# Performance work log

Measured on AMD Instinct MI355X. Metric: run time of the kernel, lower is better.

Reference implementation:

```python
import jax, jax.numpy as jnp
import numpy as np

B, T, C = 2, 2048, 2048
H, KV, D = 16, 4, 128   # n_head, n_kv_head, head_dim
EPS = 1.1920929e-07     # torch.finfo(float32).eps, F.rms_norm default


def setup_inputs() -> dict:
    key = jax.random.key(0)
    ks = jax.random.split(key, 7)
    x = jax.random.normal(ks[0], (B, T, C), dtype=jnp.float32)
    # rope angles: cos/sin of positions, broadcastable to [B,T,H,D//2]
    inv_freq = 1.0 / (10000.0 ** (jnp.arange(0, D // 2, dtype=jnp.float32) / (D // 2)))
    ang = jnp.arange(T, dtype=jnp.float32)[:, None] * inv_freq[None, :]
    cos = jnp.cos(ang)[None, :, None, :]  # [1,T,1,D/2]
    sin = jnp.sin(ang)[None, :, None, :]
    s = 0.02
    Wq = jax.random.normal(ks[1], (C, H * D), dtype=jnp.float32) * s
    Wk = jax.random.normal(ks[2], (C, KV * D), dtype=jnp.float32) * s
    Wv = jax.random.normal(ks[3], (C, KV * D), dtype=jnp.float32) * s
    Wo = jax.random.normal(ks[4], (C, C), dtype=jnp.float32) * s
    return {"x": x, "cos": cos, "sin": sin, "Wq": Wq, "Wk": Wk, "Wv": Wv, "Wo": Wo}


def _rope(t, cos, sin):
    d = t.shape[-1] // 2
    t1, t2 = t[..., :d], t[..., d:]
    return jnp.concatenate([t1 * cos + t2 * sin, -t1 * sin + t2 * cos], axis=-1)


def _rmsnorm(t):
    return t * jax.lax.rsqrt(jnp.mean(t * t, axis=-1, keepdims=True) + EPS)


def reference(x, cos, sin, Wq, Wk, Wv, Wo):
    q = (x @ Wq).reshape(B, T, H, D)
    k = (x @ Wk).reshape(B, T, KV, D)
    v = (x @ Wv).reshape(B, T, KV, D)
    q = _rmsnorm(_rope(q, cos, sin))
    k = _rmsnorm(_rope(k, cos, sin))
    # [B, KV, G, T, D] query grouped per kv head (GQA)
    G = H // KV
    qh = q.transpose(0, 2, 1, 3).reshape(B, KV, G, T, D)
    kh = k.transpose(0, 2, 1, 3)  # [B, KV, T, D]
    vh = v.transpose(0, 2, 1, 3)
    scale = 1.0 / np.sqrt(D).astype(np.float32)
    scores = jnp.einsum('bhgqd,bhkd->bhgqk', qh, kh) * scale
    causal = jnp.tril(jnp.ones((T, T), dtype=bool))
    scores = jnp.where(causal, scores, jnp.finfo(scores.dtype).min)
    attn = jax.nn.softmax(scores, axis=-1)
    y = jnp.einsum('bhgqk,bhkd->bhgqd', attn, vh)  # [B,KV,G,T,D]
    y = y.reshape(B, H, T, D).transpose(0, 2, 1, 3).reshape(B, T, C)
    return y @ Wo
```

## Files before the change

### kernel.cpp

```cpp
#include <hip/hip_runtime.h>

using bf16x8 = __attribute__((ext_vector_type(8))) short;
using f32x4  = __attribute__((ext_vector_type(4))) float;

#define B_  2
#define T_  2048
#define C_  2048
#define H_  16
#define KV_ 4
#define D_  128

__device__ __forceinline__ unsigned short f2b(float f) {
  union { float f; unsigned int u; } v; v.f = f;
  unsigned int r = v.u + 0x7fffu + ((v.u >> 16) & 1u);
  return (unsigned short)(r >> 16);
}
__device__ __forceinline__ float b2f(unsigned short u) {
  union { unsigned int u; float f; } v; v.u = ((unsigned int)u) << 16;
  return v.f;
}
__device__ __forceinline__ unsigned int cvt_pk_bf16(float lo, float hi) {
  unsigned int r;
  asm("v_cvt_pk_bf16_f32 %0, %1, %2" : "=v"(r) : "v"(lo), "v"(hi));
  return r;
}
__device__ __forceinline__ void gld_lds16(const void* g, void* l) {
  __builtin_amdgcn_global_load_lds(
      (__attribute__((address_space(1))) void*)g,
      (__attribute__((address_space(3))) void*)l, 16, 0, 0);
}

__global__ void cast_bf16_k(const float* __restrict__ in, unsigned short* __restrict__ out) {
  int i = blockIdx.x * 256 + threadIdx.x;
  float4 f = ((const float4*)in)[i];
  ushort4 u; u.x = f2b(f.x); u.y = f2b(f.y); u.z = f2b(f.z); u.w = f2b(f.w);
  ((ushort4*)out)[i] = u;
}

__global__ void wtrans4(const float* __restrict__ Wq, const float* __restrict__ Wk,
                        const float* __restrict__ Wv, const float* __restrict__ Wo,
                        unsigned short* __restrict__ Wqt, unsigned short* __restrict__ Wkt,
                        unsigned short* __restrict__ Wvt, unsigned short* __restrict__ Wot) {
  __shared__ float s[32][33];
  int id = blockIdx.x;
  const float* W; unsigned short* Wt; int N;
  if (id < 4096)      { W = Wq; Wt = Wqt; N = 2048; }
  else if (id < 5120) { W = Wk; Wt = Wkt; N = 512;  id -= 4096; }
  else if (id < 6144) { W = Wv; Wt = Wvt; N = 512;  id -= 5120; }
  else                { W = Wo; Wt = Wot; N = 2048; id -= 6144; }
  int ntiles = N >> 5;
  int n0 = (id % ntiles) * 32, k0 = (id / ntiles) * 32;
  int tx = threadIdx.x, ty = threadIdx.y;
  #pragma unroll
  for (int yy = 0; yy < 32; yy += 8)
    s[ty + yy][tx] = W[(size_t)(k0 + ty + yy) * N + n0 + tx];
  __syncthreads();
  #pragma unroll
  for (int yy = 0; yy < 32; yy += 8)
    Wt[(size_t)(n0 + ty + yy) * 2048 + k0 + tx] = f2b(s[tx][ty + yy]);
}

template <bool OUT_BF16>
__device__ __forceinline__ void gemm_tile(
    const unsigned short* __restrict__ A, const unsigned short* __restrict__ Bt,
    void* __restrict__ Cv, int K, int ldc, int m0, int n0b, int n0c,
    unsigned short* sA, unsigned short* sB)
{
  const int tid  = threadIdx.x;
  const int lane = tid & 63, w = tid >> 6;
  const int quad = lane >> 4, l16 = lane & 15;
  const int wm = (w >> 1) * 64, wn = (w & 1) * 64;

  f32x4 acc[4][4] = {};

  const unsigned short* Abase = A  + (size_t)m0  * K;
  const unsigned short* Bbase = Bt + (size_t)n0b * K;

  for (int k0 = 0; k0 < K; k0 += 32) {
    #pragma unroll
    for (int r = 0; r < 2; ++r) {
      int c = tid + r * 256;
      int row = c >> 2, col = (c & 3) * 8;
      gld_lds16(Abase + (size_t)row * K + k0 + col, sA + c * 8);
      gld_lds16(Bbase + (size_t)row * K + k0 + col, sB + c * 8);
    }
    __syncthreads();
    bf16x8 af[4], bfr[4];
    #pragma unroll
    for (int i = 0; i < 4; ++i)
      af[i]  = *(const bf16x8*)(sA + (wm + i * 16 + l16) * 32 + quad * 8);
    #pragma unroll
    for (int j = 0; j < 4; ++j)
      bfr[j] = *(const bf16x8*)(sB + (wn + j * 16 + l16) * 32 + quad * 8);
    #pragma unroll
    for (int i = 0; i < 4; ++i)
      #pragma unroll
      for (int j = 0; j < 4; ++j)
        acc[i][j] = __builtin_amdgcn_mfma_f32_16x16x32_bf16(af[i], bfr[j], acc[i][j], 0, 0, 0);
    __syncthreads();
  }
  #pragma unroll
  for (int i = 0; i < 4; ++i) {
    #pragma unroll
    for (int r = 0; r < 4; ++r) {
      int row = m0 + wm + i * 16 + quad * 4 + r;
      #pragma unroll
      for (int j = 0; j < 4; ++j) {
        int col = n0c + wn + j * 16 + l16;
        float v = acc[i][j][r];
        if (OUT_BF16) ((unsigned short*)Cv)[(size_t)row * ldc + col] = f2b(v);
        else          ((float*)Cv)[(size_t)row * ldc + col] = v;
      }
    }
  }
}

__global__ void out_gemm(const unsigned short* __restrict__ yb,
                         const unsigned short* __restrict__ Wot,
                         float* __restrict__ out) {
  __shared__ unsigned short sA[128 * 32], sB[128 * 32];
  gemm_tile<false>(yb, Wot, out, C_, C_, blockIdx.y * 128, blockIdx.x * 128, blockIdx.x * 128,
                   sA, sB);
}

__global__ __launch_bounds__(512, 2) void qkv_gemm8(
    const unsigned short* __restrict__ xb,
    const unsigned short* __restrict__ Wqt,
    const unsigned short* __restrict__ Wkt,
    const unsigned short* __restrict__ Wvt,
    unsigned short* __restrict__ q, unsigned short* __restrict__ k,
    unsigned short* __restrict__ v) {
  __shared__ unsigned short lds[65536];

  const int id  = (int)blockIdx.x;
  const int xcd = id & 7, jj = id >> 3;
  const int mt  = xcd * 2 + jj / 12;
  const int nt  = jj % 12;

  const unsigned short* Bt; unsigned short* Cp; int n0, ldc;
  if (nt < 8)       { Bt = Wqt; Cp = q; n0 = nt * 256;        ldc = 2048; }
  else if (nt < 10) { Bt = Wkt; Cp = k; n0 = (nt - 8) * 256;  ldc = 512;  }
  else              { Bt = Wvt; Cp = v; n0 = (nt - 10) * 256; ldc = 512;  }
  const int m0 = mt * 256;

  const int tid = (int)threadIdx.x;
  const int w = tid >> 6, lane = tid & 63;
  const int quad = lane >> 4, l16 = lane & 15;
  const int wr = w >> 2, wc = w & 3;
  const int swz = (l16 & 12) << 1;

  const unsigned short* Ab = xb + (size_t)m0 * 2048;
  const unsigned short* Bb = Bt + (size_t)n0 * 2048;

  const int c0 = tid, c1 = tid + 512;
  const int r0 = c0 >> 2, r1 = c1 >> 2;
  const int x0 = ((c0 & 3) * 8) ^ (((c0 >> 4) & 3) << 3);
  const int x1 = ((c1 & 3) * 8) ^ (((c1 >> 4) & 3) << 3);

#define STAGE_A(buf, kh, kb) do { \
    unsigned short* d_ = lds + (buf) * 16384 + (kh) * 8192; \
    gld_lds16(Ab + (size_t)r0 * 2048 + (kb) + (kh) * 32 + x0, d_ + c0 * 8); \
    gld_lds16(Ab + (size_t)r1 * 2048 + (kb) + (kh) * 32 + x1, d_ + c1 * 8); \
  } while (0)
#define STAGE_B(buf, kh, kb) do { \
    unsigned short* d_ = lds + 32768 + (buf) * 16384 + (kh) * 8192; \
    gld_lds16(Bb + (size_t)r0 * 2048 + (kb) + (kh) * 32 + x0, d_ + c0 * 8); \
    gld_lds16(Bb + (size_t)r1 * 2048 + (kb) + (kh) * 32 + x1, d_ + c1 * 8); \
  } while (0)

  f32x4 acc[8][4] = {};

  STAGE_A(0, 0, 0); STAGE_B(0, 0, 0); STAGE_A(0, 1, 0); STAGE_B(0, 1, 0);
  asm volatile("s_waitcnt vmcnt(4)" ::: "memory");
  __builtin_amdgcn_s_barrier();

  const unsigned short* aLd = lds + (wr * 128 + l16) * 32 + (quad * 8 ^ swz);
  const unsigned short* bLd = lds + 32768 + (wc * 64 + l16) * 32 + (quad * 8 ^ swz);

  for (int t = 0; t < 32; ++t) {
    const int cur = t & 1, nxt = cur ^ 1;
    const bool more = (t < 31);
    const int kb = (t + 1) * 64;
    const int off = cur * 16384;
    bf16x8 a[8], bbr[4];

    #pragma unroll
    for (int m = 0; m < 8; ++m) a[m] = *(const bf16x8*)(aLd + off + m * 512);
    #pragma unroll
    for (int n = 0; n < 4; ++n) bbr[n] = *(const bf16x8*)(bLd + off + n * 512);
    if (more) {
      STAGE_A(nxt, 0, kb); STAGE_B(nxt, 0, kb);
      STAGE_A(nxt, 1, kb); STAGE_B(nxt, 1, kb);
    }
    asm volatile("s_waitcnt lgkmcnt(0)" ::: "memory");
    __builtin_amdgcn_sched_barrier(0);
    __builtin_amdgcn_s_setprio(1);
    #pragma unroll
    for (int m = 0; m < 8; ++m)
      #pragma unroll
      for (int n = 0; n < 4; ++n)
        acc[m][n] = __builtin_amdgcn_mfma_f32_16x16x32_bf16(a[m], bbr[n], acc[m][n], 0, 0, 0);
    __builtin_amdgcn_s_setprio(0);
    if (more) asm volatile("s_waitcnt vmcnt(8)" ::: "memory");
    else      asm volatile("s_waitcnt vmcnt(0)" ::: "memory");
    __builtin_amdgcn_s_barrier();

    #pragma unroll
    for (int m = 0; m < 8; ++m) a[m] = *(const bf16x8*)(aLd + off + 8192 + m * 512);
    #pragma unroll
    for (int n = 0; n < 4; ++n) bbr[n] = *(const bf16x8*)(bLd + off + 8192 + n * 512);
    asm volatile("s_waitcnt lgkmcnt(0)" ::: "memory");
    __builtin_amdgcn_sched_barrier(0);
    __builtin_amdgcn_s_setprio(1);
    #pragma unroll
    for (int m = 0; m < 8; ++m)
      #pragma unroll
      for (int n = 0; n < 4; ++n)
        acc[m][n] = __builtin_amdgcn_mfma_f32_16x16x32_bf16(a[m], bbr[n], acc[m][n], 0, 0, 0);
    __builtin_amdgcn_s_setprio(0);
    if (more) asm volatile("s_waitcnt vmcnt(4)" ::: "memory");
    else      asm volatile("s_waitcnt vmcnt(0)" ::: "memory");
    __builtin_amdgcn_s_barrier();
  }
#undef STAGE_A
#undef STAGE_B

  #pragma unroll
  for (int m = 0; m < 8; ++m)
    #pragma unroll
    for (int r = 0; r < 4; ++r) {
      int row = m0 + wr * 128 + m * 16 + quad * 4 + r;
      #pragma unroll
      for (int n = 0; n < 4; ++n) {
        int col = n0 + wc * 64 + n * 16 + l16;
        Cp[(size_t)row * ldc + col] = f2b(acc[m][n][r]);
      }
    }
}

template <int NH>
__global__ void ropenorm(const unsigned short* __restrict__ in,
                         const float* __restrict__ cs, const float* __restrict__ sn,
                         unsigned short* __restrict__ out, float oscale) {
  int row  = blockIdx.x * 4 + (threadIdx.x >> 6);
  int lane = threadIdx.x & 63;
  int head = row % NH;
  int t = (row / NH) & (T_ - 1);
  int b = row / (NH * T_);
  const unsigned short* p = in + (size_t)row * D_;
  unsigned int u  = *(const unsigned int*)(p + 2 * lane);
  unsigned int up = (unsigned int)__shfl_xor((int)u, 32, 64);
  int dh = (lane & 31) * 2;
  float2 c2 = ((const float2*)(cs + t * 64))[lane & 31];
  float2 s2 = ((const float2*)(sn + t * 64))[lane & 31];
  float a0 = b2f((unsigned short)(u & 0xffff)),  a1 = b2f((unsigned short)(u >> 16));
  float p0 = b2f((unsigned short)(up & 0xffff)), p1 = b2f((unsigned short)(up >> 16));
  float sgn = (lane < 32) ? 1.0f : -1.0f;
  float oa = a0 * c2.x + sgn * p0 * s2.x;
  float ob = a1 * c2.y + sgn * p1 * s2.y;
  float ss = oa * oa + ob * ob;
  #pragma unroll
  for (int off = 32; off > 0; off >>= 1) ss += __shfl_xor(ss, off, 64);
  float r = rsqrtf(ss * (1.0f / 128.0f) + 1.1920929e-07f) * oscale;
  unsigned int outu = cvt_pk_bf16(oa * r, ob * r);
  size_t base = ((size_t)((b * NH + head) * 128 + (t >> 4))) * 2048 + (size_t)(t & 15) * 8;
  int f = ((lane < 32) ? 0 : 8) + (dh >> 3);
  *(unsigned int*)(out + base + (size_t)f * 128 + (dh & 7)) = outu;
}

__global__ void vfrag_k(const unsigned short* __restrict__ v, unsigned short* __restrict__ vf) {
  int it = blockIdx.x;
  int b = blockIdx.y >> 2, kv = blockIdx.y & 3;
  int d = threadIdx.x, ty = threadIdx.y;
  int t0 = it * 64;
  size_t obase = ((size_t)((b * KV_ + kv) * 32 + it)) * 8192
               + (size_t)(d >> 4) * 1024 + (size_t)(d & 15) * 8;
  #pragma unroll
  for (int tcg = 0; tcg < 4; ++tcg) {
    int tc = ty * 4 + tcg;
    unsigned short val[8];
    #pragma unroll
    for (int e = 0; e < 8; ++e)
      val[e] = v[(((size_t)(b * T_) + t0 + tc * 8 + e) * KV_ + kv) * D_ + d];
    ushort4 u0 = {val[0], val[1], val[2], val[3]};
    ushort4 u1 = {val[4], val[5], val[6], val[7]};
    *(ushort4*)(vf + obase + (size_t)tc * 128)     = u0;
    *(ushort4*)(vf + obase + (size_t)tc * 128 + 4) = u1;
  }
}

__global__ __launch_bounds__(256, 2) void attn_kernel(
    const unsigned short* __restrict__ qf, const unsigned short* __restrict__ kf,
    const unsigned short* __restrict__ vf, unsigned short* __restrict__ yb) {
  __shared__ __align__(16) char smem[34048];

  const int xp = (int)blockIdx.x;
  const int b = xp >> 2, kv = xp & 3;
  const int yp = (int)blockIdx.y;
  const int j = yp >> 2, hp = yp & 3;
  const int tid = threadIdx.x;
  const int w = tid >> 6, lane = tid & 63;
  const int quad = lane >> 4, l16 = lane & 15;
  const int qsel = w & 1, half = w >> 1;
  const int qt = qsel ? (63 - j) : j;
  const int h = kv * 4 + hp;
  const int q0 = qt * 32;
  const int ntile = (qt >> 1) + 1;
  unsigned short* myP = (unsigned short*)smem + w * (32 * 72);

  const unsigned short* Qf = qf + ((size_t)(b * H_ + h) * 128 + qt * 2) * 2048;
  const unsigned short* Kf = kf + (size_t)(b * KV_ + kv) * 128 * 2048;
  const unsigned short* Vf = vf + (size_t)(b * KV_ + kv) * 32 * 8192;

  bf16x8 bq[2][4];
  #pragma unroll
  for (int i = 0; i < 2; ++i)
    #pragma unroll
    for (int kk = 0; kk < 4; ++kk)
      bq[i][kk] = *(const bf16x8*)(Qf + (size_t)i * 2048 + (kk * 4 + quad) * 128 + l16 * 8);

  float l_i[2] = {0.f, 0.f};
  f32x4 o[2][8] = {};

  for (int it = half; it < ntile; it += 2) {
    const int t0 = it * 64;
    const unsigned short* Kt = Kf + (size_t)(it * 4) * 2048;
    const unsigned short* Vt = Vf + (size_t)it * 8192;

    f32x4 sc[4][2] = {};
    #pragma unroll
    for (int kk = 0; kk < 4; ++kk) {
      bf16x8 ak[4];
      #pragma unroll
      for (int jt = 0; jt < 4; ++jt)
        ak[jt] = *(const bf16x8*)(Kt + (size_t)jt * 2048 + (kk * 4 + quad) * 128 + l16 * 8);
      #pragma unroll
      for (int jt = 0; jt < 4; ++jt)
        #pragma unroll
        for (int i = 0; i < 2; ++i)
          sc[jt][i] = __builtin_amdgcn_mfma_f32_16x16x32_bf16(ak[jt], bq[i][kk], sc[jt][i], 0, 0, 0);
    }

    bf16x8 bv[2][8];
    #pragma unroll
    for (int kk2 = 0; kk2 < 2; ++kk2)
      #pragma unroll
      for (int jj = 0; jj < 8; ++jj)
        bv[kk2][jj] = *(const bf16x8*)(Vt + (size_t)jj * 1024 + (kk2 * 4 + quad) * 128 + l16 * 8);

    if (it == ntile - 1) {
      #pragma unroll
      for (int jt = 0; jt < 4; ++jt) {
        int kg = t0 + jt * 16 + quad * 4;
        #pragma unroll
        for (int i = 0; i < 2; ++i) {
          int qg = q0 + i * 16 + l16;
          #pragma unroll
          for (int r = 0; r < 4; ++r)
            if (kg + r > qg) sc[jt][i][r] = -3.0e38f;
        }
      }
    }

    #pragma unroll
    for (int i = 0; i < 2; ++i) {
      float part = 0.f;
      #pragma unroll
      for (int jt = 0; jt < 4; ++jt)
        #pragma unroll
        for (int r = 0; r < 4; ++r) {
          float p = __expf(sc[jt][i][r] - 12.0f);
          sc[jt][i][r] = p; part += p;
        }
      l_i[i] += part;
    }

    #pragma unroll
    for (int i = 0; i < 2; ++i)
      #pragma unroll
      for (int jt = 0; jt < 4; ++jt) {
        uint2 uu;
        uu.x = cvt_pk_bf16(sc[jt][i][0], sc[jt][i][1]);
        uu.y = cvt_pk_bf16(sc[jt][i][2], sc[jt][i][3]);
        *(uint2*)(myP + (i * 16 + l16) * 72 + jt * 16 + quad * 4) = uu;
      }

    #pragma unroll
    for (int kk2 = 0; kk2 < 2; ++kk2) {
      bf16x8 ap[2];
      #pragma unroll
      for (int i = 0; i < 2; ++i)
        ap[i] = *(const bf16x8*)(myP + (i * 16 + l16) * 72 + kk2 * 32 + quad * 8);
      #pragma unroll
      for (int i = 0; i < 2; ++i)
        #pragma unroll
        for (int jj = 0; jj < 8; ++jj)
          o[i][jj] = __builtin_amdgcn_mfma_f32_16x16x32_bf16(ap[i], bv[kk2][jj], o[i][jj], 0, 0, 0);
    }
  }

  float lsum[2];
  #pragma unroll
  for (int i = 0; i < 2; ++i) {
    float l = l_i[i];
    l += __shfl_xor(l, 16, 64);
    l += __shfl_xor(l, 32, 64);
    lsum[i] = l;
  }

  __syncthreads();
  float* oc = (float*)smem + qsel * (32 * 132);
  float* lc = (float*)smem + 2 * (32 * 132) + qsel * 32;
  if (half == 1) {
    #pragma unroll
    for (int i = 0; i < 2; ++i) {
      if (quad == 0) lc[i * 16 + l16] = lsum[i];
      #pragma unroll
      for (int jj = 0; jj < 8; ++jj)
        #pragma unroll
        for (int r = 0; r < 4; ++r)
          oc[(i * 16 + quad * 4 + r) * 132 + jj * 16 + l16] = o[i][jj][r];
    }
  }
  __syncthreads();
  if (half == 0) {
    #pragma unroll
    for (int i = 0; i < 2; ++i) {
      float l = lsum[i] + lc[i * 16 + l16];
      float linv = 1.0f / l;
      float lr[4];
      #pragma unroll
      for (int r = 0; r < 4; ++r) lr[r] = __shfl(linv, quad * 4 + r, 64);
      #pragma unroll
      for (int r = 0; r < 4; ++r) {
        int tg = q0 + i * 16 + quad * 4 + r;
        unsigned short* yr = yb + (((size_t)(b * T_ + tg)) * H_ + h) * D_;
        #pragma unroll
        for (int jj = 0; jj < 8; ++jj) {
          float vsum = o[i][jj][r] + oc[(i * 16 + quad * 4 + r) * 132 + jj * 16 + l16];
          yr[jj * 16 + l16] = f2b(vsum * lr[r]);
        }
      }
    }
  }
}

extern "C" void kernel_launch(void* const* d_in, const int* in_sizes, int n_in,
                              void* d_out, int out_size, void* d_ws, size_t ws_size,
                              hipStream_t stream) {
  (void)in_sizes; (void)n_in; (void)out_size; (void)ws_size;
  const float* x  = (const float*)d_in[0];
  const float* cs = (const float*)d_in[1];
  const float* sn = (const float*)d_in[2];
  const float* Wq = (const float*)d_in[3];
  const float* Wk = (const float*)d_in[4];
  const float* Wv = (const float*)d_in[5];
  const float* Wo = (const float*)d_in[6];
  float* out = (float*)d_out;
  char* ws = (char*)d_ws;

  unsigned short* xb   = (unsigned short*)(ws + 0);
  unsigned short* Wqt  = (unsigned short*)(ws + 16777216);
  unsigned short* Wkt  = (unsigned short*)(ws + 25165824);
  unsigned short* Wvt  = (unsigned short*)(ws + 27262976);
  unsigned short* Wot  = (unsigned short*)(ws + 29360128);
  unsigned short* qraw = (unsigned short*)(ws + 37748736);
  unsigned short* kraw = (unsigned short*)(ws + 54525952);
  unsigned short* vraw = (unsigned short*)(ws + 58720256);
  unsigned short* qfr  = (unsigned short*)(ws + 62914560);
  unsigned short* kfr  = (unsigned short*)(ws + 79691776);
  unsigned short* vfr  = (unsigned short*)(ws + 83886080);
  unsigned short* yb   = qraw;

  cast_bf16_k<<<dim3(8192), dim3(256), 0, stream>>>(x, xb);
  wtrans4<<<dim3(10240), dim3(32, 8), 0, stream>>>(Wq, Wk, Wv, Wo, Wqt, Wkt, Wvt, Wot);
  qkv_gemm8<<<dim3(192), dim3(512), 0, stream>>>(xb, Wqt, Wkt, Wvt, qraw, kraw, vraw);
  ropenorm<16><<<dim3(16384), dim3(256), 0, stream>>>(qraw, cs, sn, qfr, 0.08838834764831845f);
  ropenorm<4><<<dim3(4096),  dim3(256), 0, stream>>>(kraw, cs, sn, kfr, 1.0f);
  vfrag_k<<<dim3(32, 8), dim3(128, 2), 0, stream>>>(vraw, vfr);
  attn_kernel<<<dim3(8, 128), dim3(256), 0, stream>>>(qfr, kfr, vfr, yb);
  out_gemm<<<dim3(16, 32), dim3(256), 0, stream>>>(yb, Wot, out);
}
```

Measured before the change: 318.9 us.

## Fuse QKV weights into one GEMM with 256x192 tiles over 256 blocks

Packs Wq, Wk and Wv transposes contiguously and runs a single QKV GEMM with 256x192 tiles, giving 256 blocks (one full wave on the CUs) instead of 192. The output is one interleaved [B*T, 3072] buffer, so ropenorm and vfrag_k now take a leading dimension and offset. The k-loop is also simplified from hand-tuned split waitcnt/setprio scheduling to a plain double buffer with __syncthreads. This may lose some of the load/compute overlap the manual scheduling provided.

```diff
diff --git a/kernel.cpp b/kernel.cpp
--- a/kernel.cpp
+++ b/kernel.cpp
@@ -123,117 +123,97 @@
                    sA, sB);
 }
 
-__global__ __launch_bounds__(512, 2) void qkv_gemm8(
+__global__ __launch_bounds__(512, 2) void qkv_gemm2p(
     const unsigned short* __restrict__ xb,
-    const unsigned short* __restrict__ Wqt,
-    const unsigned short* __restrict__ Wkt,
-    const unsigned short* __restrict__ Wvt,
-    unsigned short* __restrict__ q, unsigned short* __restrict__ k,
-    unsigned short* __restrict__ v) {
-  __shared__ unsigned short lds[65536];
+    const unsigned short* __restrict__ Wt,
+    unsigned short* __restrict__ qkv) {
+  __shared__ unsigned short lds[57344];
 
   const int id  = (int)blockIdx.x;
-  const int xcd = id & 7, jj = id >> 3;
-  const int mt  = xcd * 2 + jj / 12;
-  const int nt  = jj % 12;
-
-  const unsigned short* Bt; unsigned short* Cp; int n0, ldc;
-  if (nt < 8)       { Bt = Wqt; Cp = q; n0 = nt * 256;        ldc = 2048; }
-  else if (nt < 10) { Bt = Wkt; Cp = k; n0 = (nt - 8) * 256;  ldc = 512;  }
-  else              { Bt = Wvt; Cp = v; n0 = (nt - 10) * 256; ldc = 512;  }
-  const int m0 = mt * 256;
+  const int xcd = id & 7, j = id >> 3;
+  const int mt  = xcd * 2 + (j >> 4);
+  const int nt  = j & 15;
+  const int m0 = mt * 256, n0 = nt * 192;
 
   const int tid = (int)threadIdx.x;
   const int w = tid >> 6, lane = tid & 63;
   const int quad = lane >> 4, l16 = lane & 15;
-  const int wr = w >> 2, wc = w & 3;
+  const int wr = w >> 1, wc = w & 1;
   const int swz = (l16 & 12) << 1;
 
   const unsigned short* Ab = xb + (size_t)m0 * 2048;
-  const unsigned short* Bb = Bt + (size_t)n0 * 2048;
-
-  const int c0 = tid, c1 = tid + 512;
-  const int r0 = c0 >> 2, r1 = c1 >> 2;
-  const int x0 = ((c0 & 3) * 8) ^ (((c0 >> 4) & 3) << 3);
-  const int x1 = ((c1 & 3) * 8) ^ (((c1 >> 4) & 3) << 3);
-
-#define STAGE_A(buf, kh, kb) do { \
-    unsigned short* d_ = lds + (buf) * 16384 + (kh) * 8192; \
-    gld_lds16(Ab + (size_t)r0 * 2048 + (kb) + (kh) * 32 + x0, d_ + c0 * 8); \
-    gld_lds16(Ab + (size_t)r1 * 2048 + (kb) + (kh) * 32 + x1, d_ + c1 * 8); \
+  const unsigned short* Bb = Wt + (size_t)n0 * 2048;
+
+  int ar[4], axc[4];
+  #pragma unroll
+  for (int kq = 0; kq < 4; ++kq) {
+    int ca = tid + kq * 512;
+    ar[kq]  = (ca & 1023) >> 2;
+    axc[kq] = ((ca & 3) * 8) ^ ((((ca & 1023) >> 4) & 3) << 3);
+  }
+  const int khb1 = (tid < 256) ? 0 : 1;
+  int bidx[3] = { tid, tid + 512 - khb1 * 768, tid + 256 };
+  int bkh[3]  = { 0, khb1, 1 };
+  int br[3], bxc[3];
+  #pragma unroll
+  for (int kq = 0; kq < 3; ++kq) {
+    br[kq]  = bidx[kq] >> 2;
+    bxc[kq] = ((bidx[kq] & 3) * 8) ^ (((bidx[kq] >> 4) & 3) << 3);
+  }
+
+#define STAGE(buf, kb) do { \
+    unsigned short* da_ = lds + (buf) * 16384; \
+    _Pragma("unroll") \
+    for (int kq = 0; kq < 4; ++kq) { \
+      int ca_ = tid + kq * 512; \
+      gld_lds16(Ab + (size_t)ar[kq] * 2048 + (kb) + (ca_ >> 10) * 32 + axc[kq], da_ + ca_ * 8); \
+    } \
+    unsigned short* db_ = lds + 32768 + (buf) * 12288; \
+    _Pragma("unroll") \
+    for (int kq = 0; kq < 3; ++kq) \
+      gld_lds16(Bb + (size_t)br[kq] * 2048 + (kb) + bkh[kq] * 32 + bxc[kq], \
+                db_ + bkh[kq] * 6144 + bidx[kq] * 8); \
   } while (0)
-#define STAGE_B(buf, kh, kb) do { \
-    unsigned short* d_ = lds + 32768 + (buf) * 16384 + (kh) * 8192; \
-    gld_lds16(Bb + (size_t)r0 * 2048 + (kb) + (kh) * 32 + x0, d_ + c0 * 8); \
-    gld_lds16(Bb + (size_t)r1 * 2048 + (kb) + (kh) * 32 + x1, d_ + c1 * 8); \
-  } while (0)
-
-  f32x4 acc[8][4] = {};
-
-  STAGE_A(0, 0, 0); STAGE_B(0, 0, 0); STAGE_A(0, 1, 0); STAGE_B(0, 1, 0);
-  asm volatile("s_waitcnt vmcnt(4)" ::: "memory");
-  __builtin_amdgcn_s_barrier();
-
-  const unsigned short* aLd = lds + (wr * 128 + l16) * 32 + (quad * 8 ^ swz);
-  const unsigned short* bLd = lds + 32768 + (wc * 64 + l16) * 32 + (quad * 8 ^ swz);
+
+  f32x4 acc[4][6] = {};
+
+  STAGE(0, 0);
+  __syncthreads();
+
+  const unsigned short* aB = lds + (wr * 64 + l16) * 32 + (quad * 8 ^ swz);
+  const unsigned short* bB = lds + 32768 + (wc * 96 + l16) * 32 + (quad * 8 ^ swz);
 
   for (int t = 0; t < 32; ++t) {
-    const int cur = t & 1, nxt = cur ^ 1;
-    const bool more = (t < 31);
-    const int kb = (t + 1) * 64;
-    const int off = cur * 16384;
-    bf16x8 a[8], bbr[4];
-
-    #pragma unroll
-    for (int m = 0; m < 8; ++m) a[m] = *(const bf16x8*)(aLd + off + m * 512);
-    #pragma unroll
-    for (int n = 0; n < 4; ++n) bbr[n] = *(const bf16x8*)(bLd + off + n * 512);
-    if (more) {
-      STAGE_A(nxt, 0, kb); STAGE_B(nxt, 0, kb);
-      STAGE_A(nxt, 1, kb); STAGE_B(nxt, 1, kb);
-    }
-    asm volatile("s_waitcnt lgkmcnt(0)" ::: "memory");
-    __builtin_amdgcn_sched_barrier(0);
-    __builtin_amdgcn_s_setprio(1);
-    #pragma unroll
-    for (int m = 0; m < 8; ++m)
-      #pragma unroll
-      for (int n = 0; n < 4; ++n)
-        acc[m][n] = __builtin_amdgcn_mfma_f32_16x16x32_bf16(a[m], bbr[n], acc[m][n], 0, 0, 0);
-    __builtin_amdgcn_s_setprio(0);
-    if (more) asm volatile("s_waitcnt vmcnt(8)" ::: "memory");
-    else      asm volatile("s_waitcnt vmcnt(0)" ::: "memory");
-    __builtin_amdgcn_s_barrier();
-
-    #pragma unroll
-    for (int m = 0; m < 8; ++m) a[m] = *(const bf16x8*)(aLd + off + 8192 + m * 512);
-    #pragma unroll
-    for (int n = 0; n < 4; ++n) bbr[n] = *(const bf16x8*)(bLd + off + 8192 + n * 512);
-    asm volatile("s_waitcnt lgkmcnt(0)" ::: "memory");
-    __builtin_amdgcn_sched_barrier(0);
-    __builtin_amdgcn_s_setprio(1);
-    #pragma unroll
-    for (int m = 0; m < 8; ++m)
-      #pragma unroll
-      for (int n = 0; n < 4; ++n)
-        acc[m][n] = __builtin_amdgcn_mfma_f32_16x16x32_bf16(a[m], bbr[n], acc[m][n], 0, 0, 0);
-    __builtin_amdgcn_s_setprio(0);
-    if (more) asm volatile("s_waitcnt vmcnt(4)" ::: "memory");
-    else      asm volatile("s_waitcnt vmcnt(0)" ::: "memory");
-    __builtin_amdgcn_s_barrier();
-  }
-#undef STAGE_A
-#undef STAGE_B
-
-  #pragma unroll
-  for (int m = 0; m < 8; ++m)
+    const int cur = t & 1;
+    if (t < 31) STAGE(cur ^ 1, (t + 1) * 64);
+    #pragma unroll
+    for (int kh = 0; kh < 2; ++kh) {
+      bf16x8 a[4], b[6];
+      #pragma unroll
+      for (int m = 0; m < 4; ++m)
+        a[m] = *(const bf16x8*)(aB + cur * 16384 + kh * 8192 + m * 512);
+      #pragma unroll
+      for (int n = 0; n < 6; ++n)
+        b[n] = *(const bf16x8*)(bB + cur * 12288 + kh * 6144 + n * 512);
+      #pragma unroll
+      for (int m = 0; m < 4; ++m)
+        #pragma unroll
+        for (int n = 0; n < 6; ++n)
+          acc[m][n] = __builtin_amdgcn_mfma_f32_16x16x32_bf16(a[m], b[n], acc[m][n], 0, 0, 0);
+    }
+    __syncthreads();
+  }
+#undef STAGE
+
+  #pragma unroll
+  for (int m = 0; m < 4; ++m)
     #pragma unroll
     for (int r = 0; r < 4; ++r) {
-      int row = m0 + wr * 128 + m * 16 + quad * 4 + r;
-      #pragma unroll
-      for (int n = 0; n < 4; ++n) {
-        int col = n0 + wc * 64 + n * 16 + l16;
-        Cp[(size_t)row * ldc + col] = f2b(acc[m][n][r]);
+      int row = m0 + wr * 64 + m * 16 + quad * 4 + r;
+      #pragma unroll
+      for (int n = 0; n < 6; ++n) {
+        int col = n0 + wc * 96 + n * 16 + l16;
+        qkv[(size_t)row * 3072 + col] = f2b(acc[m][n][r]);
       }
     }
 }
@@ -241,13 +221,13 @@
 template <int NH>
 __global__ void ropenorm(const unsigned short* __restrict__ in,
                          const float* __restrict__ cs, const float* __restrict__ sn,
-                         unsigned short* __restrict__ out, float oscale) {
+                         unsigned short* __restrict__ out, float oscale, int ld, int off) {
   int row  = blockIdx.x * 4 + (threadIdx.x >> 6);
   int lane = threadIdx.x & 63;
   int head = row % NH;
   int t = (row / NH) & (T_ - 1);
   int b = row / (NH * T_);
-  const unsigned short* p = in + (size_t)row * D_;
+  const unsigned short* p = in + (size_t)(b * T_ + t) * ld + off + head * D_;
   unsigned int u  = *(const unsigned int*)(p + 2 * lane);
   unsigned int up = (unsigned int)__shfl_xor((int)u, 32, 64);
   int dh = (lane & 31) * 2;
@@ -260,7 +240,7 @@
   float ob = a1 * c2.y + sgn * p1 * s2.y;
   float ss = oa * oa + ob * ob;
   #pragma unroll
-  for (int off = 32; off > 0; off >>= 1) ss += __shfl_xor(ss, off, 64);
+  for (int off2 = 32; off2 > 0; off2 >>= 1) ss += __shfl_xor(ss, off2, 64);
   float r = rsqrtf(ss * (1.0f / 128.0f) + 1.1920929e-07f) * oscale;
   unsigned int outu = cvt_pk_bf16(oa * r, ob * r);
   size_t base = ((size_t)((b * NH + head) * 128 + (t >> 4))) * 2048 + (size_t)(t & 15) * 8;
@@ -268,7 +248,7 @@
   *(unsigned int*)(out + base + (size_t)f * 128 + (dh & 7)) = outu;
 }
 
-__global__ void vfrag_k(const unsigned short* __restrict__ v, unsigned short* __restrict__ vf) {
+__global__ void vfrag_k(const unsigned short* __restrict__ qkv, unsigned short* __restrict__ vf) {
   int it = blockIdx.x;
   int b = blockIdx.y >> 2, kv = blockIdx.y & 3;
   int d = threadIdx.x, ty = threadIdx.y;
@@ -281,7 +261,7 @@
     unsigned short val[8];
     #pragma unroll
     for (int e = 0; e < 8; ++e)
-      val[e] = v[(((size_t)(b * T_) + t0 + tc * 8 + e) * KV_ + kv) * D_ + d];
+      val[e] = qkv[((size_t)(b * T_) + t0 + tc * 8 + e) * 3072 + 2560 + kv * D_ + d];
     ushort4 u0 = {val[0], val[1], val[2], val[3]};
     ushort4 u1 = {val[4], val[5], val[6], val[7]};
     *(ushort4*)(vf + obase + (size_t)tc * 128)     = u0;
@@ -459,25 +439,24 @@
   float* out = (float*)d_out;
   char* ws = (char*)d_ws;
 
-  unsigned short* xb   = (unsigned short*)(ws + 0);
-  unsigned short* Wqt  = (unsigned short*)(ws + 16777216);
-  unsigned short* Wkt  = (unsigned short*)(ws + 25165824);
-  unsigned short* Wvt  = (unsigned short*)(ws + 27262976);
-  unsigned short* Wot  = (unsigned short*)(ws + 29360128);
-  unsigned short* qraw = (unsigned short*)(ws + 37748736);
-  unsigned short* kraw = (unsigned short*)(ws + 54525952);
-  unsigned short* vraw = (unsigned short*)(ws + 58720256);
-  unsigned short* qfr  = (unsigned short*)(ws + 62914560);
-  unsigned short* kfr  = (unsigned short*)(ws + 79691776);
-  unsigned short* vfr  = (unsigned short*)(ws + 83886080);
-  unsigned short* yb   = qraw;
+  unsigned short* xb     = (unsigned short*)(ws + 0);
+  unsigned short* Wqkvt  = (unsigned short*)(ws + 16777216);
+  unsigned short* Wot    = (unsigned short*)(ws + 29360128);
+  unsigned short* qkvcat = (unsigned short*)(ws + 37748736);
+  unsigned short* qfr    = (unsigned short*)(ws + 62914560);
+  unsigned short* kfr    = (unsigned short*)(ws + 79691776);
+  unsigned short* vfr    = (unsigned short*)(ws + 83886080);
+  unsigned short* yb     = xb;
 
   cast_bf16_k<<<dim3(8192), dim3(256), 0, stream>>>(x, xb);
-  wtrans4<<<dim3(10240), dim3(32, 8), 0, stream>>>(Wq, Wk, Wv, Wo, Wqt, Wkt, Wvt, Wot);
-  qkv_gemm8<<<dim3(192), dim3(512), 0, stream>>>(xb, Wqt, Wkt, Wvt, qraw, kraw, vraw);
-  ropenorm<16><<<dim3(16384), dim3(256), 0, stream>>>(qraw, cs, sn, qfr, 0.08838834764831845f);
-  ropenorm<4><<<dim3(4096),  dim3(256), 0, stream>>>(kraw, cs, sn, kfr, 1.0f);
-  vfrag_k<<<dim3(32, 8), dim3(128, 2), 0, stream>>>(vraw, vfr);
+  wtrans4<<<dim3(10240), dim3(32, 8), 0, stream>>>(
+      Wq, Wk, Wv, Wo,
+      Wqkvt, Wqkvt + (size_t)2048 * 2048, Wqkvt + (size_t)2560 * 2048, Wot);
+  qkv_gemm2p<<<dim3(256), dim3(512), 0, stream>>>(xb, Wqkvt, qkvcat);
+  ropenorm<16><<<dim3(16384), dim3(256), 0, stream>>>(qkvcat, cs, sn, qfr,
+                                                      0.08838834764831845f, 3072, 0);
+  ropenorm<4><<<dim3(4096),  dim3(256), 0, stream>>>(qkvcat, cs, sn, kfr, 1.0f, 3072, 2048);
+  vfrag_k<<<dim3(32, 8), dim3(128, 2), 0, stream>>>(qkvcat, vfr);
   attn_kernel<<<dim3(8, 128), dim3(256), 0, stream>>>(qfr, kfr, vfr, yb);
   out_gemm<<<dim3(16, 32), dim3(256), 0, stream>>>(yb, Wot, out);
 }
```

Measured after the change: 306.8 us. 3.8% less time.
